# Optimization experiments

Hardware: AMD Instinct MI355X
Metric: run time of the kernel (lower is better)

## Reference

```python
import math
import jax, jax.numpy as jnp
import numpy as np

MAX_LEN = 1024

def _sinusoidal_pe(seq_len, d_model):
    pos = jnp.arange(seq_len, dtype=jnp.float32)[:, None]
    div = jnp.exp(jnp.arange(0, d_model, 2, dtype=jnp.float32) * (-math.log(10000.0) / d_model))
    ang = pos * div  # [S, D/2]
    pe = jnp.zeros((seq_len, d_model), dtype=jnp.float32)
    pe = pe.at[:, 0::2].set(jnp.sin(ang))
    pe = pe.at[:, 1::2].set(jnp.cos(ang))
    return pe

def setup_inputs() -> dict:
    key = jax.random.key(0)
    ks = jax.random.split(key, 4)
    B, S, D, H = 4, 1024, 1024, 16
    x = jax.random.normal(ks[0], (B, S, D), dtype=jnp.float32)
    gamma = jnp.ones((D,), dtype=jnp.float32)
    beta = jnp.zeros((D,), dtype=jnp.float32)
    w_pos = jax.random.normal(ks[1], (2 * D, D), dtype=jnp.float32) * (1.0 / math.sqrt(D))
    w_tok = jax.random.normal(ks[2], (3 * D, D), dtype=jnp.float32) * (1.0 / math.sqrt(D))
    bias_table = jax.random.normal(ks[3], (2 * MAX_LEN, H), dtype=jnp.float32) * 0.02
    return {"x": x, "gamma": gamma, "beta": beta, "w_pos": w_pos, "w_tok": w_tok, "bias_table": bias_table}

def reference(x, gamma, beta, w_pos, w_tok, bias_table):
    B, S, D = x.shape
    H = bias_table.shape[1]
    dh = D // H
    scale = 1.0 / math.sqrt(2 * dh)

    # untied positional scores (identical across batch)
    pe = _sinusoidal_pe(S, D)                      # [S, D]
    pos = pe @ w_pos.T                             # [S, 2D]
    pos_k, pos_q = pos[:, :D], pos[:, D:]
    pos_k = pos_k.reshape(S, H, dh)
    pos_q = pos_q.reshape(S, H, dh)
    pos_attn = jnp.einsum('qhd,khd->hqk', pos_q, pos_k)  # [H, S, S]

    # token scores
    mu = jnp.mean(x, axis=-1, keepdims=True)
    var = jnp.mean((x - mu) ** 2, axis=-1, keepdims=True)
    xn = (x - mu) / jnp.sqrt(var + 1e-5) * gamma + beta
    tok = xn @ w_tok.T                             # [B, S, 3D]
    tok_k, tok_q, tok_v = jnp.split(tok, 3, axis=-1)
    tok_k = tok_k.reshape(B, S, H, dh)
    tok_q = tok_q.reshape(B, S, H, dh)
    tok_v = tok_v.reshape(B, S, H, dh)
    tok_attn = jnp.einsum('bqhd,bkhd->bhqk', tok_q, tok_k)  # [B, H, S, S]

    attn = (tok_attn + pos_attn[None]) / scale

    # relative-position bias
    rel = jnp.arange(S)[None, :] - jnp.arange(S)[:, None] + MAX_LEN  # [S, S]
    bias = bias_table[rel]                         # [S, S, H]
    attn = attn + jnp.transpose(bias, (2, 0, 1))[None]

    attn = jax.nn.softmax(attn, axis=-1)
    out = jnp.einsum('bhqk,bkhd->bqhd', attn, tok_v)
    return out.reshape(B, S, D)
```

## Files before the change

kernel.cpp:

```cpp
#include <hip/hip_runtime.h>
#include <math.h>

#define SB 1024
#define DM 1024
#define BB 4
#define NH 16
#define DH 64
#define ML 1024

typedef __attribute__((ext_vector_type(8))) short short8;
typedef __attribute__((ext_vector_type(8))) _Float16 half8;
typedef __attribute__((ext_vector_type(4))) float f32x4;
typedef unsigned short u16;

__device__ __forceinline__ u16 f2bf(float x) {
  unsigned u = __float_as_uint(x);
  u += 0x7fffu + ((u >> 16) & 1u);
  return (u16)(u >> 16);
}
__device__ __forceinline__ float bf2f(u16 h) { return __uint_as_float((unsigned)h << 16); }

__device__ __forceinline__ void async16(void* lds, const void* g) {
  __builtin_amdgcn_global_load_lds(
      (const __attribute__((address_space(1))) unsigned*)g,
      (__attribute__((address_space(3))) unsigned*)lds, 16, 0, 0);
}


__device__ __forceinline__ void pack16_body(int rt, int t, const float* __restrict__ src,
    _Float16* __restrict__ dH, _Float16* __restrict__ dL, float scale) {
  int r16 = t >> 4, ks = t & 15;
  const float* sp = src + (size_t)(rt * 16 + r16) * 1024 + ks * 64;
  float v[64];
  #pragma unroll
  for (int i = 0; i < 16; ++i) {
    float4 f = *(const float4*)(sp + i * 4);
    v[i*4+0] = f.x; v[i*4+1] = f.y; v[i*4+2] = f.z; v[i*4+3] = f.w;
  }
  #pragma unroll
  for (int hf = 0; hf < 2; ++hf) {
    int kt = ks * 2 + hf;
    #pragma unroll
    for (int gg = 0; gg < 4; ++gg) {
      half8 hv, lv;
      #pragma unroll
      for (int j = 0; j < 8; ++j) {
        float x = v[hf * 32 + gg * 8 + j] * scale;
        _Float16 h = (_Float16)x;
        hv[j] = h;
        lv[j] = (_Float16)(x - (float)h);
      }
      size_t off = ((size_t)(rt * 32 + kt) * 64 + r16 + gg * 16) * 8;
      *(half8*)(dH + off) = hv;
      *(half8*)(dL + off) = lv;
    }
  }
}

__device__ __forceinline__ void pe_pack_body(int rt, int t,
    _Float16* __restrict__ dH, _Float16* __restrict__ dL) {
  int r16 = t >> 4, ks = t & 15;
  int p = rt * 16 + r16;
  float v[64];
  #pragma unroll
  for (int i = 0; i < 32; ++i) {
    int c0 = ks * 64 + 2 * i;
    float div = expf((float)c0 * (-9.210340371976184f / (float)DM));
    float ang = (float)p * div;
    v[2*i]   = sinf(ang);
    v[2*i+1] = cosf(ang);
  }
  #pragma unroll
  for (int hf = 0; hf < 2; ++hf) {
    int kt = ks * 2 + hf;
    #pragma unroll
    for (int gg = 0; gg < 4; ++gg) {
      half8 hv, lv;
      #pragma unroll
      for (int j = 0; j < 8; ++j) {
        float x = v[hf * 32 + gg * 8 + j];
        _Float16 h = (_Float16)x;
        hv[j] = h;
        lv[j] = (_Float16)(x - (float)h);
      }
      size_t off = ((size_t)(rt * 32 + kt) * 64 + r16 + gg * 16) * 8;
      *(half8*)(dH + off) = hv;
      *(half8*)(dL + off) = lv;
    }
  }
}

__device__ __forceinline__ void ln_pack_body(int rt, int t, const float* __restrict__ x,
    const float* __restrict__ gamma, const float* __restrict__ beta,
    _Float16* __restrict__ dH, _Float16* __restrict__ dL) {
  int r16 = t >> 4, ks = t & 15;
  const float* sp = x + (size_t)(rt * 16 + r16) * 1024 + ks * 64;
  float v[64];
  float s1 = 0.f, s2 = 0.f;
  #pragma unroll
  for (int i = 0; i < 16; ++i) {
    float4 f = *(const float4*)(sp + i * 4);
    v[i*4+0] = f.x; v[i*4+1] = f.y; v[i*4+2] = f.z; v[i*4+3] = f.w;
    s1 += f.x + f.y + f.z + f.w;
    s2 += f.x*f.x + f.y*f.y + f.z*f.z + f.w*f.w;
  }
  #pragma unroll
  for (int off = 1; off < 16; off <<= 1) {
    s1 += __shfl_xor(s1, off, 64);
    s2 += __shfl_xor(s2, off, 64);
  }
  float mu = s1 * (1.0f / 1024.0f);
  float var = s2 * (1.0f / 1024.0f) - mu * mu;
  float rstd = rsqrtf(var + 1e-5f);
  #pragma unroll
  for (int hf = 0; hf < 2; ++hf) {
    int kt = ks * 2 + hf;
    #pragma unroll
    for (int gg = 0; gg < 4; ++gg) {
      const float* gp = gamma + ks * 64 + hf * 32 + gg * 8;
      const float* bp = beta  + ks * 64 + hf * 32 + gg * 8;
      half8 hv, lv;
      #pragma unroll
      for (int j = 0; j < 8; ++j) {
        float xn = (v[hf * 32 + gg * 8 + j] - mu) * rstd * gp[j] + bp[j];
        _Float16 h = (_Float16)xn;
        hv[j] = h;
        lv[j] = (_Float16)(xn - (float)h);
      }
      size_t off = ((size_t)(rt * 32 + kt) * 64 + r16 + gg * 16) * 8;
      *(half8*)(dH + off) = hv;
      *(half8*)(dL + off) = lv;
    }
  }
}

__global__ __launch_bounds__(256) void prep_all(
    const float* __restrict__ x, const float* __restrict__ gamma,
    const float* __restrict__ beta,
    const float* __restrict__ w_pos, const float* __restrict__ w_tok,
    _Float16* __restrict__ peH, _Float16* __restrict__ peL,
    _Float16* __restrict__ xnH, _Float16* __restrict__ xnL,
    _Float16* __restrict__ wpH, _Float16* __restrict__ wpL,
    _Float16* __restrict__ wtH, _Float16* __restrict__ wtL) {
  int bid = blockIdx.x;
  int t = threadIdx.x;
  if (bid < 64)       pe_pack_body(bid, t, peH, peL);
  else if (bid < 320) ln_pack_body(bid - 64, t, x, gamma, beta, xnH, xnL);
  else if (bid < 448) pack16_body(bid - 320, t, w_pos, wpH, wpL, 32.0f);
  else                pack16_body(bid - 448, t, w_tok, wtH, wtL, 32.0f);
}

#define GBM 128
#define GBN 256

__global__ __launch_bounds__(256, 2) void gemm16p(
    const _Float16* __restrict__ AtH, const _Float16* __restrict__ AtL,
    const _Float16* __restrict__ ApH, const _Float16* __restrict__ ApL,
    const _Float16* __restrict__ BtH, const _Float16* __restrict__ BtL,
    const _Float16* __restrict__ BpH, const _Float16* __restrict__ BpL,
    u16* __restrict__ KtfH, u16* __restrict__ KtfL,
    u16* __restrict__ KpfH, u16* __restrict__ KpfL,
    u16* __restrict__ QH, u16* __restrict__ QL,
    u16* __restrict__ pQH, u16* __restrict__ pQL,
    u16* __restrict__ vF, float sK, float sQ, float sV) {
  __shared__ _Float16 L[32 * 512];
  int t = threadIdx.x;
  int wv = t >> 6, lane = t & 63;
  int wm = wv >> 1, wn = wv & 1;
  int r16 = lane & 15, g = lane >> 4;

  int bid = blockIdx.x;
  bool isPos = (bid >= 384);
  int idx = isPos ? bid - 384 : bid;
  int n0, m0;
  const _Float16 *AH, *AL, *BH, *BL;
  if (isPos) { n0 = (idx & 7) * 256;  m0 = (idx >> 3) * 128;
               AH = ApH; AL = ApL; BH = BpH; BL = BpL; }
  else       { n0 = (idx % 12) * 256; m0 = (idx / 12) * 128;
               AH = AtH; AL = AtL; BH = BtH; BL = BtL; }
  int mt0 = m0 >> 4, nt0 = n0 >> 4;
  bool split = isPos || (n0 < 2048);

  f32x4 acc[4][8];
  #pragma unroll
  for (int i = 0; i < 4; ++i)
    #pragma unroll
    for (int j = 0; j < 8; ++j) acc[i][j] = (f32x4){0.f, 0.f, 0.f, 0.f};

  for (int kt = 0; kt < 32; ++kt) {
    __syncthreads();
    #pragma unroll
    for (int rd = 0; rd < 8; ++rd) {
      int ci = rd * 4 + wv;
      bool isAlo = (ci < 16) && (ci & 1);
      if (!split && isAlo) continue;
      const _Float16* src;
      if (ci < 16) {
        int mt = ci >> 1, pl = ci & 1;
        const _Float16* P = pl ? AL : AH;
        src = P + ((size_t)((mt0 + mt) * 32 + kt) * 64 + lane) * 8;
      } else {
        int nt = ci - 16;
        src = BH + ((size_t)((nt0 + nt) * 32 + kt) * 64 + lane) * 8;
      }
      async16(&L[ci * 512], src);
    }
    half8 blo[8];
    if (split) {
      #pragma unroll
      for (int j = 0; j < 8; ++j) {
        int ntg = nt0 + wn * 8 + j;
        blo[j] = *(const half8*)(BL + ((size_t)(ntg * 32 + kt) * 64 + lane) * 8);
      }
    }
    __syncthreads();

    half8 ah[4], al[4];
    #pragma unroll
    for (int i = 0; i < 4; ++i)
      ah[i] = *(const half8*)&L[(((wm * 4 + i) * 2 + 0) * 512) + lane * 8];
    if (split) {
      #pragma unroll
      for (int i = 0; i < 4; ++i)
        al[i] = *(const half8*)&L[(((wm * 4 + i) * 2 + 1) * 512) + lane * 8];
    }
    #pragma unroll
    for (int j = 0; j < 8; ++j) {
      half8 bh = *(const half8*)&L[((16 + wn * 8 + j) * 512) + lane * 8];
      #pragma unroll
      for (int i = 0; i < 4; ++i) {
        acc[i][j] = __builtin_amdgcn_mfma_f32_16x16x32_f16(ah[i], bh, acc[i][j], 0, 0, 0);
        if (split) {
          acc[i][j] = __builtin_amdgcn_mfma_f32_16x16x32_f16(al[i], bh, acc[i][j], 0, 0, 0);
          acc[i][j] = __builtin_amdgcn_mfma_f32_16x16x32_f16(ah[i], blo[j], acc[i][j], 0, 0, 0);
        }
      }
    }
  }

  int band = n0 >> 10;
  u16* fKH = isPos ? KpfH : KtfH;
  u16* fKL = isPos ? KpfL : KtfL;
  u16* qHo = isPos ? pQH  : QH;
  u16* qLo = isPos ? pQL  : QL;
  if (band == 1) {
    #pragma unroll
    for (int i = 0; i < 4; ++i)
      #pragma unroll
      for (int j = 0; j < 8; ++j) {
        int lc = (n0 & 1023) + wn * 128 + j * 16 + r16;
        #pragma unroll
        for (int reg = 0; reg < 4; ++reg) {
          int row = m0 + wm * 64 + i * 16 + g * 4 + reg;
          float cv = acc[i][j][reg] * sQ;
          u16 hi = f2bf(cv);
          qHo[(size_t)row * 1024 + lc] = hi;
          qLo[(size_t)row * 1024 + lc] = f2bf(cv - bf2f(hi));
        }
      }
  } else if (band == 0) {
    #pragma unroll
    for (int i = 0; i < 4; ++i)
      #pragma unroll
      for (int j = 0; j < 8; ++j) {
        int colg = n0 + wn * 128 + j * 16 + r16;
        int h = colg >> 6, dc = colg & 63;
        #pragma unroll
        for (int reg = 0; reg < 4; ++reg) {
          int row = m0 + wm * 64 + i * 16 + g * 4 + reg;
          int bhK = (row >> 10) * NH + h;
          size_t a = ((size_t)((bhK * 64 + ((row & 1023) >> 4)) * 2 + (dc >> 5)) << 9)
                   + ((row & 15) + 16 * ((dc >> 3) & 3)) * 8 + (dc & 7);
          float cv = acc[i][j][reg] * sK;
          u16 hi = f2bf(cv);
          fKH[a] = hi;
          fKL[a] = f2bf(cv - bf2f(hi));
        }
      }
  } else {
    #pragma unroll
    for (int i = 0; i < 4; ++i)
      #pragma unroll
      for (int j = 0; j < 8; ++j) {
        int colg = (n0 & 1023) + wn * 128 + j * 16 + r16;
        int h = colg >> 6, dc = colg & 63;
        #pragma unroll
        for (int reg = 0; reg < 4; ++reg) {
          int row = m0 + wm * 64 + i * 16 + g * 4 + reg;
          int s = row & 1023;
          size_t a = ((size_t)((((row >> 10) * NH + h) * 32 + (s >> 5)) * 4 + (dc >> 4)) << 9)
                   + ((s >> 3) & 3) * 128 + (s & 7) + (dc & 15) * 8;
          vF[a] = f2bf(acc[i][j][reg] * sV);
        }
      }
  }
}

__global__ __launch_bounds__(256, 2) void gemm16m(
    const _Float16* __restrict__ AtH, const _Float16* __restrict__ AtL,
    const _Float16* __restrict__ ApH, const _Float16* __restrict__ ApL,
    const float* __restrict__ Wt, const float* __restrict__ Wp,
    u16* __restrict__ KtfH, u16* __restrict__ KtfL,
    u16* __restrict__ KpfH, u16* __restrict__ KpfL,
    u16* __restrict__ QH, u16* __restrict__ QL,
    u16* __restrict__ pQH, u16* __restrict__ pQL,
    u16* __restrict__ vF, float sK, float sQ, float sV) {
  __shared__ _Float16 L[48 * 512];
  int t = threadIdx.x;
  int wv = t >> 6, lane = t & 63;
  int wm = wv >> 1, wn = wv & 1;
  int r16 = lane & 15, g = lane >> 4;

  int bid = blockIdx.x;
  bool isPos = (bid >= 384);
  int idx = isPos ? bid - 384 : bid;
  int n0, m0;
  const _Float16 *AH, *AL;
  const float* W;
  if (isPos) { n0 = (idx & 7) * 256;  m0 = (idx >> 3) * 128; AH = ApH; AL = ApL; W = Wp; }
  else       { n0 = (idx % 12) * 256; m0 = (idx / 12) * 128; AH = AtH; AL = AtL; W = Wt; }
  int mt0 = m0 >> 4, nt0 = n0 >> 4;
  bool split = isPos || (n0 < 2048);

  f32x4 acc[4][8];
  #pragma unroll
  for (int i = 0; i < 4; ++i)
    #pragma unroll
    for (int j = 0; j < 8; ++j) acc[i][j] = (f32x4){0.f, 0.f, 0.f, 0.f};

  for (int kt = 0; kt < 32; ++kt) {
    __syncthreads();
    #pragma unroll
    for (int rd = 0; rd < 4; ++rd) {
      int ci = rd * 4 + wv;
      int mt = ci >> 1, pl = ci & 1;
      if (!split && pl) continue;
      const _Float16* src = (pl ? AL : AH)
          + ((size_t)((mt0 + mt) * 32 + kt) * 64 + lane) * 8;
      async16(&L[ci * 512], src);
    }
    #pragma unroll
    for (int tt = 0; tt < 4; ++tt) {
      int nt = wv * 4 + tt;
      const float* wsrc = W + (size_t)((nt0 + nt) * 16 + r16) * 1024 + kt * 32 + g * 8;
      float4 w0 = *(const float4*)wsrc;
      float4 w1 = *(const float4*)(wsrc + 4);
      float wvv[8] = {w0.x, w0.y, w0.z, w0.w, w1.x, w1.y, w1.z, w1.w};
      half8 hv, lv;
      #pragma unroll
      for (int j = 0; j < 8; ++j) {
        float xx = wvv[j] * 32.0f;
        _Float16 h = (_Float16)xx;
        hv[j] = h;
        lv[j] = (_Float16)(xx - (float)h);
      }
      *(half8*)&L[(16 + nt) * 512 + lane * 8] = hv;
      if (split) *(half8*)&L[(32 + nt) * 512 + lane * 8] = lv;
    }
    __syncthreads();

    half8 ah[4], al[4];
    #pragma unroll
    for (int i = 0; i < 4; ++i)
      ah[i] = *(const half8*)&L[(((wm * 4 + i) * 2 + 0) * 512) + lane * 8];
    if (split) {
      #pragma unroll
      for (int i = 0; i < 4; ++i)
        al[i] = *(const half8*)&L[(((wm * 4 + i) * 2 + 1) * 512) + lane * 8];
    }
    #pragma unroll
    for (int j = 0; j < 8; ++j) {
      half8 bh = *(const half8*)&L[((16 + wn * 8 + j) * 512) + lane * 8];
      #pragma unroll
      for (int i = 0; i < 4; ++i) {
        acc[i][j] = __builtin_amdgcn_mfma_f32_16x16x32_f16(ah[i], bh, acc[i][j], 0, 0, 0);
        if (split) {
          half8 bl = *(const half8*)&L[((32 + wn * 8 + j) * 512) + lane * 8];
          acc[i][j] = __builtin_amdgcn_mfma_f32_16x16x32_f16(al[i], bh, acc[i][j], 0, 0, 0);
          acc[i][j] = __builtin_amdgcn_mfma_f32_16x16x32_f16(ah[i], bl, acc[i][j], 0, 0, 0);
        }
      }
    }
  }

  int band = n0 >> 10;
  u16* fKH = isPos ? KpfH : KtfH;
  u16* fKL = isPos ? KpfL : KtfL;
  u16* qHo = isPos ? pQH  : QH;
  u16* qLo = isPos ? pQL  : QL;
  if (band == 1) {
    #pragma unroll
    for (int i = 0; i < 4; ++i)
      #pragma unroll
      for (int j = 0; j < 8; ++j) {
        int lc = (n0 & 1023) + wn * 128 + j * 16 + r16;
        #pragma unroll
        for (int reg = 0; reg < 4; ++reg) {
          int row = m0 + wm * 64 + i * 16 + g * 4 + reg;
          float cv = acc[i][j][reg] * sQ;
          u16 hi = f2bf(cv);
          qHo[(size_t)row * 1024 + lc] = hi;
          qLo[(size_t)row * 1024 + lc] = f2bf(cv - bf2f(hi));
        }
      }
  } else if (band == 0) {
    #pragma unroll
    for (int i = 0; i < 4; ++i)
      #pragma unroll
      for (int j = 0; j < 8; ++j) {
        int colg = n0 + wn * 128 + j * 16 + r16;
        int h = colg >> 6, dc = colg & 63;
        #pragma unroll
        for (int reg = 0; reg < 4; ++reg) {
          int row = m0 + wm * 64 + i * 16 + g * 4 + reg;
          int bhK = (row >> 10) * NH + h;
          size_t a = ((size_t)((bhK * 64 + ((row & 1023) >> 4)) * 2 + (dc >> 5)) << 9)
                   + ((row & 15) + 16 * ((dc >> 3) & 3)) * 8 + (dc & 7);
          float cv = acc[i][j][reg] * sK;
          u16 hi = f2bf(cv);
          fKH[a] = hi;
          fKL[a] = f2bf(cv - bf2f(hi));
        }
      }
  } else {
    #pragma unroll
    for (int i = 0; i < 4; ++i)
      #pragma unroll
      for (int j = 0; j < 8; ++j) {
        int colg = (n0 & 1023) + wn * 128 + j * 16 + r16;
        int h = colg >> 6, dc = colg & 63;
        #pragma unroll
        for (int reg = 0; reg < 4; ++reg) {
          int row = m0 + wm * 64 + i * 16 + g * 4 + reg;
          int s = row & 1023;
          size_t a = ((size_t)((((row >> 10) * NH + h) * 32 + (s >> 5)) * 4 + (dc >> 4)) << 9)
                   + ((s >> 3) & 3) * 128 + (s & 7) + (dc & 15) * 8;
          vF[a] = f2bf(acc[i][j][reg] * sV);
        }
      }
  }
}

__global__ __launch_bounds__(256, 2) void attn_mfma9(
    const u16* __restrict__ KtfH, const u16* __restrict__ KtfL,
    const u16* __restrict__ KpfH, const u16* __restrict__ KpfL,
    const u16* __restrict__ QHg, const u16* __restrict__ QLg,
    const u16* __restrict__ pQH, const u16* __restrict__ pQL,
    const u16* __restrict__ Vf,
    const float* __restrict__ bt,
    float* __restrict__ out) {
  __shared__ u16 Pb[4][2][16 * 72];
  __shared__ float biasL[2 * ML];
  int bid = blockIdx.x;
  int qt = bid & 7;
  int bh = bid >> 3;
  int b = bh >> 4, h = bh & 15;
  int q0 = qt * 128;
  int t = threadIdx.x;
  int wv = t >> 6, lane = t & 63;
  int g = lane >> 4, r16 = lane & 15;

  #pragma unroll
  for (int k = 0; k < 8; ++k)
    biasL[t + k * 256] = bt[(size_t)(t + k * 256) * NH + h];

  short8 qhi[2][4], qlo[2][4];
  #pragma unroll
  for (int cc = 0; cc < 2; ++cc) {
    int qrow = q0 + wv * 32 + cc * 16 + r16;
    #pragma unroll
    for (int c = 0; c < 4; ++c) {
      if (c < 2) {
        size_t off = (size_t)(b * SB + qrow) * 1024 + h * DH + c * 32 + g * 8;
        qhi[cc][c] = *(const short8*)(QHg + off);
        qlo[cc][c] = *(const short8*)(QLg + off);
      } else {
        size_t off = (size_t)qrow * 1024 + h * DH + (c - 2) * 32 + g * 8;
        qhi[cc][c] = *(const short8*)(pQH + off);
        qlo[cc][c] = *(const short8*)(pQL + off);
      }
    }
  }
  __syncthreads();

  f32x4 O[2][4];
  #pragma unroll
  for (int cc = 0; cc < 2; ++cc)
    #pragma unroll
    for (int dt = 0; dt < 4; ++dt) O[cc][dt] = (f32x4){0.f, 0.f, 0.f, 0.f};
  float m_run[2][4], l_run[2][4];
  #pragma unroll
  for (int cc = 0; cc < 2; ++cc)
    #pragma unroll
    for (int reg = 0; reg < 4; ++reg) { m_run[cc][reg] = -3e38f; l_run[cc][reg] = 0.f; }

  int qb0 = q0 + wv * 32 + g * 4;
  const u16* ktH = KtfH + (size_t)(bh * 64) * 1024 + lane * 8;
  const u16* ktL = KtfL + (size_t)(bh * 64) * 1024 + lane * 8;
  const u16* kpH = KpfH + (size_t)(h * 64) * 1024 + lane * 8;
  const u16* kpL = KpfL + (size_t)(h * 64) * 1024 + lane * 8;
  const u16* vp  = Vf + (size_t)(bh * 32) * 2048 + lane * 8;
  int bb = ML + r16 - qb0;

  for (int ktr = 0; ktr < 16; ++ktr) {
    float bias[2][4][4];
    #pragma unroll
    for (int nt = 0; nt < 4; ++nt)
      #pragma unroll
      for (int reg = 0; reg < 4; ++reg) {
        bias[0][nt][reg] = biasL[bb + nt * 16 - reg];
        bias[1][nt][reg] = biasL[bb - 16 + nt * 16 - reg];
      }

    f32x4 S[2][4];
    #pragma unroll
    for (int nt = 0; nt < 4; ++nt) {
      f32x4 a0 = (f32x4){0.f, 0.f, 0.f, 0.f};
      f32x4 a1 = (f32x4){0.f, 0.f, 0.f, 0.f};
      #pragma unroll
      for (int c = 0; c < 4; ++c) {
        const u16* ph = (c < 2) ? ktH : kpH;
        const u16* pl = (c < 2) ? ktL : kpL;
        int co = (c < 2) ? c : (c - 2);
        short8 bhi = *(const short8*)(ph + nt * 1024 + co * 512);
        short8 blo = *(const short8*)(pl + nt * 1024 + co * 512);
        a0 = __builtin_amdgcn_mfma_f32_16x16x32_bf16(qhi[0][c], bhi, a0, 0, 0, 0);
        a1 = __builtin_amdgcn_mfma_f32_16x16x32_bf16(qhi[1][c], bhi, a1, 0, 0, 0);
        a0 = __builtin_amdgcn_mfma_f32_16x16x32_bf16(qlo[0][c], bhi, a0, 0, 0, 0);
        a1 = __builtin_amdgcn_mfma_f32_16x16x32_bf16(qlo[1][c], bhi, a1, 0, 0, 0);
        a0 = __builtin_amdgcn_mfma_f32_16x16x32_bf16(qhi[0][c], blo, a0, 0, 0, 0);
        a1 = __builtin_amdgcn_mfma_f32_16x16x32_bf16(qhi[1][c], blo, a1, 0, 0, 0);
      }
      S[0][nt] = a0; S[1][nt] = a1;
    }

    short8 vfrag[2][4];
    #pragma unroll
    for (int kc = 0; kc < 2; ++kc)
      #pragma unroll
      for (int dt = 0; dt < 4; ++dt)
        vfrag[kc][dt] = *(const short8*)(vp + (kc * 4 + dt) * 512);

    #pragma unroll
    for (int cc = 0; cc < 2; ++cc)
      #pragma unroll
      for (int nt = 0; nt < 4; ++nt)
        #pragma unroll
        for (int reg = 0; reg < 4; ++reg)
          S[cc][nt][reg] += bias[cc][nt][reg];

    float tm[2][4], al[2][4];
    #pragma unroll
    for (int cc = 0; cc < 2; ++cc)
      #pragma unroll
      for (int reg = 0; reg < 4; ++reg)
        tm[cc][reg] = fmaxf(fmaxf(S[cc][0][reg], S[cc][1][reg]),
                            fmaxf(S[cc][2][reg], S[cc][3][reg]));
    #pragma unroll
    for (int off = 1; off < 16; off <<= 1)
      #pragma unroll
      for (int cc = 0; cc < 2; ++cc)
        #pragma unroll
        for (int reg = 0; reg < 4; ++reg)
          tm[cc][reg] = fmaxf(tm[cc][reg], __shfl_xor(tm[cc][reg], off, 64));
    #pragma unroll
    for (int cc = 0; cc < 2; ++cc)
      #pragma unroll
      for (int reg = 0; reg < 4; ++reg) {
        float mn = fmaxf(m_run[cc][reg], tm[cc][reg]);
        al[cc][reg] = __expf(m_run[cc][reg] - mn);
        m_run[cc][reg] = mn;
      }
    float ts[2][4] = {{0.f, 0.f, 0.f, 0.f}, {0.f, 0.f, 0.f, 0.f}};
    #pragma unroll
    for (int cc = 0; cc < 2; ++cc)
      #pragma unroll
      for (int nt = 0; nt < 4; ++nt)
        #pragma unroll
        for (int reg = 0; reg < 4; ++reg) {
          float p = __expf(S[cc][nt][reg] - m_run[cc][reg]);
          S[cc][nt][reg] = p;
          ts[cc][reg] += p;
        }
    #pragma unroll
    for (int cc = 0; cc < 2; ++cc)
      #pragma unroll
      for (int reg = 0; reg < 4; ++reg)
        l_run[cc][reg] = l_run[cc][reg] * al[cc][reg] + ts[cc][reg];
    #pragma unroll
    for (int cc = 0; cc < 2; ++cc)
      #pragma unroll
      for (int dt = 0; dt < 4; ++dt)
        #pragma unroll
        for (int reg = 0; reg < 4; ++reg)
          O[cc][dt][reg] *= al[cc][reg];

    #pragma unroll
    for (int cc = 0; cc < 2; ++cc) {
      u16* pb = Pb[wv][cc];
      #pragma unroll
      for (int nt = 0; nt < 4; ++nt)
        #pragma unroll
        for (int reg = 0; reg < 4; ++reg)
          pb[(g * 4 + reg) * 72 + nt * 16 + r16] = f2bf(S[cc][nt][reg]);
    }

    #pragma unroll
    for (int kc = 0; kc < 2; ++kc) {
      #pragma unroll
      for (int cc = 0; cc < 2; ++cc) {
        short8 pa = *(const short8*)&Pb[wv][cc][r16 * 72 + kc * 32 + g * 8];
        #pragma unroll
        for (int dt = 0; dt < 4; ++dt)
          O[cc][dt] = __builtin_amdgcn_mfma_f32_16x16x32_bf16(pa, vfrag[kc][dt], O[cc][dt], 0, 0, 0);
      }
    }

    ktH += 4096; ktL += 4096; kpH += 4096; kpL += 4096;
    vp += 4096; bb += 64;
  }

  #pragma unroll
  for (int off = 1; off < 16; off <<= 1)
    #pragma unroll
    for (int cc = 0; cc < 2; ++cc)
      #pragma unroll
      for (int reg = 0; reg < 4; ++reg)
        l_run[cc][reg] += __shfl_xor(l_run[cc][reg], off, 64);
  #pragma unroll
  for (int cc = 0; cc < 2; ++cc)
    #pragma unroll
    for (int reg = 0; reg < 4; ++reg) l_run[cc][reg] = 1.0f / l_run[cc][reg];
  #pragma unroll
  for (int cc = 0; cc < 2; ++cc)
    #pragma unroll
    for (int dt = 0; dt < 4; ++dt)
      #pragma unroll
      for (int reg = 0; reg < 4; ++reg)
        out[(size_t)(b * SB + qb0 + cc * 16 + reg) * DM + h * DH + dt * 16 + r16] =
            O[cc][dt][reg] * l_run[cc][reg];
}

extern "C" void kernel_launch(void* const* d_in, const int* in_sizes, int n_in,
                              void* d_out, int out_size, void* d_ws, size_t ws_size,
                              hipStream_t stream) {
  const float* x     = (const float*)d_in[0];
  const float* gamma = (const float*)d_in[1];
  const float* beta  = (const float*)d_in[2];
  const float* w_pos = (const float*)d_in[3];
  const float* w_tok = (const float*)d_in[4];
  const float* bt    = (const float*)d_in[5];
  float* out = (float*)d_out;
  float* ws  = (float*)d_ws;
  const size_t M1 = 1u << 20;
  const float IS = 11.313708498984761f;

  u16 *KtfH, *KtfL, *KpfH, *KpfL, *QH, *QL, *posQH, *posQL, *Vf;

  if (ws_size >= 22 * M1 * 4) {
    _Float16* peH = (_Float16*)(ws);
    _Float16* peL = (_Float16*)(ws + M1 / 2);
    _Float16* xnH = (_Float16*)(ws + 1 * M1);
    _Float16* xnL = (_Float16*)(ws + 3 * M1);
    _Float16* wpH = (_Float16*)(ws + 5 * M1);
    _Float16* wpL = (_Float16*)(ws + 6 * M1);
    _Float16* wtH = (_Float16*)(ws + 7 * M1);
    _Float16* wtL = (_Float16*)(ws + 8 * M1 + M1/2);
    KpfH  = (u16*)(ws + 10 * M1);
    KpfL  = (u16*)(ws + 10 * M1 + M1 / 2);
    posQH = (u16*)(ws + 11 * M1);
    posQL = (u16*)(ws + 11 * M1 + M1 / 2);
    KtfH  = (u16*)(ws + 12 * M1);
    KtfL  = (u16*)(ws + 14 * M1);
    QH    = (u16*)(ws + 16 * M1);
    QL    = (u16*)(ws + 18 * M1);
    Vf    = (u16*)(ws + 20 * M1);

    prep_all<<<640, 256, 0, stream>>>(x, gamma, beta, w_pos, w_tok,
        peH, peL, xnH, xnL, wpH, wpL, wtH, wtL);
    gemm16p<<<448, 256, 0, stream>>>(
        xnH, xnL, peH, peL, wtH, wtL, wpH, wpL,
        KtfH, KtfL, KpfH, KpfL, QH, QL, posQH, posQL, Vf,
        1.0f / 32.0f, IS / 32.0f, 1.0f / 32.0f);
  } else {
    _Float16* peH = (_Float16*)(ws);
    _Float16* peL = (_Float16*)(ws + M1 / 2);
    _Float16* xnH = (_Float16*)(ws + 1 * M1);
    _Float16* xnL = (_Float16*)(ws + 3 * M1);
    KpfH  = (u16*)(ws + 5 * M1);
    KpfL  = (u16*)(ws + 5 * M1 + M1 / 2);
    posQH = (u16*)(ws + 6 * M1);
    posQL = (u16*)(ws + 6 * M1 + M1 / 2);
    KtfH  = (u16*)(ws + 7 * M1);
    KtfL  = (u16*)(ws + 9 * M1);
    QH    = (u16*)(ws + 11 * M1);
    QL    = (u16*)(ws + 13 * M1);
    Vf    = (u16*)(ws + 15 * M1);

    prep_all<<<320, 256, 0, stream>>>(x, gamma, beta, w_pos, w_tok,
        peH, peL, xnH, xnL, (_Float16*)nullptr, (_Float16*)nullptr,
        (_Float16*)nullptr, (_Float16*)nullptr);
    gemm16m<<<448, 256, 0, stream>>>(
        xnH, xnL, peH, peL, w_tok, w_pos,
        KtfH, KtfL, KpfH, KpfL, QH, QL, posQH, posQL, Vf,
        1.0f / 32.0f, IS / 32.0f, 1.0f / 32.0f);
  }

  attn_mfma9<<<BB * NH * (SB / 128), 256, 0, stream>>>(
      KtfH, KtfL, KpfH, KpfL, QH, QL, posQH, posQL, Vf, bt, out);
}
```

Baseline: 259.2 us.

## Stage K/V tiles in LDS and remap block IDs across XCDs

In the attention kernel, each K/V tile (token K hi/lo, positional K hi/lo, V) is now loaded once per block into LDS through async global-to-LDS copies and shared by all four waves. Previously every wave read the same tile straight from global memory, so the change cuts redundant global and cache traffic. The P buffer shrinks to one tile per wave and is reused for each cc pass. Block IDs in the attention and both GEMM kernels are permuted so that neighbouring logical blocks land on the same XCD, which should improve L2 locality. The cost is two barriers per iteration and a full vmcnt wait with no double buffering, so load latency is no longer overlapped with compute.

```diff
diff --git a/kernel.cpp b/kernel.cpp
--- a/kernel.cpp
+++ b/kernel.cpp
@@ -169,7 +169,8 @@
   int wm = wv >> 1, wn = wv & 1;
   int r16 = lane & 15, g = lane >> 4;
 
-  int bid = blockIdx.x;
+  int phys = blockIdx.x;
+  int bid = (phys & 7) * 56 + (phys >> 3);
   bool isPos = (bid >= 384);
   int idx = isPos ? bid - 384 : bid;
   int n0, m0;
@@ -311,7 +312,8 @@
   int wm = wv >> 1, wn = wv & 1;
   int r16 = lane & 15, g = lane >> 4;
 
-  int bid = blockIdx.x;
+  int phys = blockIdx.x;
+  int bid = (phys & 7) * 56 + (phys >> 3);
   bool isPos = (bid >= 384);
   int idx = isPos ? bid - 384 : bid;
   int n0, m0;
@@ -441,7 +443,7 @@
   }
 }
 
-__global__ __launch_bounds__(256, 2) void attn_mfma9(
+__global__ __launch_bounds__(256, 2) void attn_mfma10(
     const u16* __restrict__ KtfH, const u16* __restrict__ KtfL,
     const u16* __restrict__ KpfH, const u16* __restrict__ KpfL,
     const u16* __restrict__ QHg, const u16* __restrict__ QLg,
@@ -449,9 +451,12 @@
     const u16* __restrict__ Vf,
     const float* __restrict__ bt,
     float* __restrict__ out) {
-  __shared__ u16 Pb[4][2][16 * 72];
+  __shared__ u16 Klds[5 * 4096];
   __shared__ float biasL[2 * ML];
-  int bid = blockIdx.x;
+  __shared__ u16 Pb[4][16 * 72];
+
+  int phys = blockIdx.x;
+  int bid = (phys & 7) * 64 + (phys >> 3);
   int qt = bid & 7;
   int bh = bid >> 3;
   int b = bh >> 4, h = bh & 15;
@@ -459,6 +464,7 @@
   int t = threadIdx.x;
   int wv = t >> 6, lane = t & 63;
   int g = lane >> 4, r16 = lane & 15;
+  int lo = lane * 8;
 
   #pragma unroll
   for (int k = 0; k < 8; ++k)
@@ -481,7 +487,6 @@
       }
     }
   }
-  __syncthreads();
 
   f32x4 O[2][4];
   #pragma unroll
@@ -495,14 +500,30 @@
     for (int reg = 0; reg < 4; ++reg) { m_run[cc][reg] = -3e38f; l_run[cc][reg] = 0.f; }
 
   int qb0 = q0 + wv * 32 + g * 4;
-  const u16* ktH = KtfH + (size_t)(bh * 64) * 1024 + lane * 8;
-  const u16* ktL = KtfL + (size_t)(bh * 64) * 1024 + lane * 8;
-  const u16* kpH = KpfH + (size_t)(h * 64) * 1024 + lane * 8;
-  const u16* kpL = KpfL + (size_t)(h * 64) * 1024 + lane * 8;
-  const u16* vp  = Vf + (size_t)(bh * 32) * 2048 + lane * 8;
+  const u16* ktHb = KtfH + (size_t)(bh * 64) * 1024;
+  const u16* ktLb = KtfL + (size_t)(bh * 64) * 1024;
+  const u16* kpHb = KpfH + (size_t)(h * 64) * 1024;
+  const u16* kpLb = KpfL + (size_t)(h * 64) * 1024;
+  const u16* vb   = Vf   + (size_t)(bh * 32) * 2048;
   int bb = ML + r16 - qb0;
 
   for (int ktr = 0; ktr < 16; ++ktr) {
+    __syncthreads();
+
+    {
+      int p0 = wv * 512, p1 = (wv + 4) * 512;
+      async16(&Klds[0 * 4096 + p0], ktHb + p0 + lo);
+      async16(&Klds[0 * 4096 + p1], ktHb + p1 + lo);
+      async16(&Klds[1 * 4096 + p0], ktLb + p0 + lo);
+      async16(&Klds[1 * 4096 + p1], ktLb + p1 + lo);
+      async16(&Klds[2 * 4096 + p0], kpHb + p0 + lo);
+      async16(&Klds[2 * 4096 + p1], kpHb + p1 + lo);
+      async16(&Klds[3 * 4096 + p0], kpLb + p0 + lo);
+      async16(&Klds[3 * 4096 + p1], kpLb + p1 + lo);
+      async16(&Klds[4 * 4096 + p0], vb + p0 + lo);
+      async16(&Klds[4 * 4096 + p1], vb + p1 + lo);
+    }
+
     float bias[2][4][4];
     #pragma unroll
     for (int nt = 0; nt < 4; ++nt)
@@ -512,6 +533,9 @@
         bias[1][nt][reg] = biasL[bb - 16 + nt * 16 - reg];
       }
 
+    asm volatile("s_waitcnt vmcnt(0)" ::: "memory");
+    __syncthreads();
+
     f32x4 S[2][4];
     #pragma unroll
     for (int nt = 0; nt < 4; ++nt) {
@@ -519,11 +543,10 @@
       f32x4 a1 = (f32x4){0.f, 0.f, 0.f, 0.f};
       #pragma unroll
       for (int c = 0; c < 4; ++c) {
-        const u16* ph = (c < 2) ? ktH : kpH;
-        const u16* pl = (c < 2) ? ktL : kpL;
-        int co = (c < 2) ? c : (c - 2);
-        short8 bhi = *(const short8*)(ph + nt * 1024 + co * 512);
-        short8 blo = *(const short8*)(pl + nt * 1024 + co * 512);
+        int ch = (c < 2) ? 0 : 2;
+        int co = c & 1;
+        short8 bhi = *(const short8*)&Klds[(ch + 0) * 4096 + nt * 1024 + co * 512 + lo];
+        short8 blo = *(const short8*)&Klds[(ch + 1) * 4096 + nt * 1024 + co * 512 + lo];
         a0 = __builtin_amdgcn_mfma_f32_16x16x32_bf16(qhi[0][c], bhi, a0, 0, 0, 0);
         a1 = __builtin_amdgcn_mfma_f32_16x16x32_bf16(qhi[1][c], bhi, a1, 0, 0, 0);
         a0 = __builtin_amdgcn_mfma_f32_16x16x32_bf16(qlo[0][c], bhi, a0, 0, 0, 0);
@@ -539,7 +562,7 @@
     for (int kc = 0; kc < 2; ++kc)
       #pragma unroll
       for (int dt = 0; dt < 4; ++dt)
-        vfrag[kc][dt] = *(const short8*)(vp + (kc * 4 + dt) * 512);
+        vfrag[kc][dt] = *(const short8*)&Klds[4 * 4096 + (kc * 4 + dt) * 512 + lo];
 
     #pragma unroll
     for (int cc = 0; cc < 2; ++cc)
@@ -597,27 +620,23 @@
 
     #pragma unroll
     for (int cc = 0; cc < 2; ++cc) {
-      u16* pb = Pb[wv][cc];
+      u16* pb = Pb[wv];
       #pragma unroll
       for (int nt = 0; nt < 4; ++nt)
         #pragma unroll
         for (int reg = 0; reg < 4; ++reg)
           pb[(g * 4 + reg) * 72 + nt * 16 + r16] = f2bf(S[cc][nt][reg]);
-    }
-
-    #pragma unroll
-    for (int kc = 0; kc < 2; ++kc) {
-      #pragma unroll
-      for (int cc = 0; cc < 2; ++cc) {
-        short8 pa = *(const short8*)&Pb[wv][cc][r16 * 72 + kc * 32 + g * 8];
+      #pragma unroll
+      for (int kc = 0; kc < 2; ++kc) {
+        short8 pa = *(const short8*)&Pb[wv][r16 * 72 + kc * 32 + g * 8];
         #pragma unroll
         for (int dt = 0; dt < 4; ++dt)
           O[cc][dt] = __builtin_amdgcn_mfma_f32_16x16x32_bf16(pa, vfrag[kc][dt], O[cc][dt], 0, 0, 0);
       }
     }
 
-    ktH += 4096; ktL += 4096; kpH += 4096; kpL += 4096;
-    vp += 4096; bb += 64;
+    ktHb += 4096; ktLb += 4096; kpHb += 4096; kpLb += 4096;
+    vb += 4096; bb += 64;
   }
 
   #pragma unroll
@@ -706,6 +725,6 @@
         1.0f / 32.0f, IS / 32.0f, 1.0f / 32.0f);
   }
 
-  attn_mfma9<<<BB * NH * (SB / 128), 256, 0, stream>>>(
+  attn_mfma10<<<BB * NH * (SB / 128), 256, 0, stream>>>(
       KtfH, KtfL, KpfH, KpfL, QH, QL, posQH, posQL, Vf, bt, out);
 }
```

Result: faster. 251.7 us (-2.9%).
